# Performance work log

Hardware: AMD Instinct MI355X
Metric: run time of the kernel (lower is better)

The kernel has to match this reference:

```python
import jax, jax.numpy as jnp
import numpy as np

B, T, E, S, D, HG = 16, 1024, 1024, 256, 512, 128
P_MIN, P_MAX, K_MAX, MAX_INNOV, EPS = 1e-6, 10.0, 1.0, 10.0, 1e-6


def setup_inputs() -> dict:
    key = jax.random.key(0)
    ks = jax.random.split(key, 16)
    g = lambda k, shape, fan: jax.random.normal(k, shape, jnp.float32) * np.float32(1.0 / np.sqrt(fan))
    # orthogonal init for the state-transition matrix A
    A = jnp.linalg.qr(jax.random.normal(ks[1], (S, S), jnp.float32))[0]
    return {
        "x": jax.random.normal(ks[0], (B, T, E), jnp.float32),
        "W_in": g(ks[2], (E, D), E), "b_in": jnp.zeros((D,), jnp.float32),
        "W_state": g(ks[3], (D, S), D), "b_state": jnp.zeros((S,), jnp.float32),
        "A": A, "H": g(ks[4], (D, S), D),
        "Q": jnp.full((S,), 0.1, jnp.float32), "R": jnp.full((D,), 0.1, jnp.float32),
        "W_z": g(ks[5], (HG, HG + S), HG + S), "W_r": g(ks[6], (HG, HG + S), HG + S),
        "W_h": g(ks[7], (HG, HG + S), HG + S),
        "b_z": jnp.zeros((HG,), jnp.float32), "b_r": jnp.zeros((HG,), jnp.float32),
        "b_h": jnp.zeros((HG,), jnp.float32),
        "W_out": g(ks[8], (HG, S), HG),
        "W_outp": g(ks[9], (D, E), D), "b_outp": jnp.zeros((E,), jnp.float32),
    }


def reference(x, W_in, b_in, W_state, b_state, A, H, Q, R,
              W_z, W_r, W_h, b_z, b_r, b_h, W_out, W_outp, b_outp):
    # input projection with GELU (Dense(d_inner, activation='gelu'))
    u = jax.nn.gelu(jnp.einsum("bte,ed->btd", x, W_in) + b_in)  # [B,T,D]
    q_sp = jax.nn.softplus(Q)                 # process noise, per state dim
    r_eff = jnp.mean(jax.nn.softplus(R))      # scalar effective measurement noise

    def step(carry, u_t):
        x_est, P, h = carry                   # [B,S], [B,S], [B,HG]
        # 1. state prediction (+ learned control input from measurement)
        x_pred = x_est @ A.T + u_t @ W_state + b_state          # [B,S]
        # 2. covariance prediction with clipping
        P_pred = jnp.clip(P + q_sp, P_MIN, P_MAX)                # [B,S]
        # 3. innovation (clipped for stability)
        y = jnp.clip(u_t - x_pred @ H.T, -MAX_INNOV, MAX_INNOV)  # [B,D]
        # 4. Kalman gain, bounded in [0, k_max]
        K = jnp.clip(P_pred / (P_pred + r_eff + EPS), 0.0, K_MAX)  # [B,S]
        # 5. state update: x_post = x_pred + K * (H^T @ innovation)
        x_post = x_pred + K * (y @ H)                            # [B,S]
        # 6. covariance update
        P_post = jnp.clip(P_pred * (1.0 - K), P_MIN, P_MAX)      # [B,S]
        # GRU gating over posterior state
        hx = jnp.concatenate([h, x_post], axis=-1)               # [B,HG+S]
        zg = jax.nn.sigmoid(hx @ W_z.T + b_z)
        rg = jax.nn.sigmoid(hx @ W_r.T + b_r)
        hc = jnp.tanh(jnp.concatenate([rg * h, x_post], axis=-1) @ W_h.T + b_h)
        h_new = (1.0 - zg) * h + zg * hc                         # [B,HG]
        # neural correction of state via GRU output projection
        x_final = x_post + h_new @ W_out                         # [B,S]
        return (x_final, P_post, h_new), x_final

    x0 = jnp.zeros((x.shape[0], S), x.dtype)
    P0 = jnp.ones((x.shape[0], S), x.dtype)   # identity covariance (diagonal)
    h0 = jnp.zeros((x.shape[0], HG), x.dtype)
    (_, _, _), xs = jax.lax.scan(step, (x0, P0, h0), jnp.swapaxes(u, 0, 1))
    xs = jnp.swapaxes(xs, 0, 1)               # [B,T,S]
    obs = jnp.einsum("bts,ds->btd", xs, H)    # reconstruct observation space
    out = jnp.einsum("btd,de->bte", obs, W_outp) + b_outp
    return out + x                            # residual connection
```

## Files before the change

### kernel.cpp

```cpp
#include <hip/hip_runtime.h>
#include <cstdint>
#include <cstddef>

#define NB 16
#define NT 1024
#define NE 1024
#define NS 256
#define ND 512
#define NH 128
#define T0 16

#define OFF_US   ((size_t)0)
#define OFF_HU   ((size_t)4194304)
#define OFF_U3   ((size_t)8388608)
#define OFF_KT   ((size_t)12582912)
#define OFF_HT   ((size_t)12845056)
#define OFF_AT   ((size_t)12976128)
#define OFF_G    ((size_t)13041664)
#define OFF_IG   ((size_t)13107200)
#define OFF_MINF ((size_t)13172736)
#define OFF_WZT  ((size_t)13238272)
#define OFF_WRT  ((size_t)13287424)
#define OFF_WHT  ((size_t)13336576)
#define OFF_HTWO ((size_t)13385728)
#define OFF_PACK ((size_t)13647872)
#define OFF_XSPK ((size_t)14360576)

#define PK_A   0
#define PK_G   65536
#define PK_M   131072
#define PK_Z   196608
#define PK_R   245760
#define PK_H   294912
#define PK_O   344064
#define PK_WIN 376832
#define PK_WST 901120
#define PK_HM  1032192
#define PK_HTW 1163264


typedef short bf16x8 __attribute__((ext_vector_type(8)));
typedef float f32x4 __attribute__((ext_vector_type(4)));
typedef unsigned int u32x2 __attribute__((ext_vector_type(2)));

#define MFMA(a, b, c) __builtin_amdgcn_mfma_f32_16x16x32_bf16((a), (b), (c), 0, 0, 0)

#define SYNCW() do { \
    __builtin_amdgcn_sched_barrier(0); \
    asm volatile("s_waitcnt lgkmcnt(0)" ::: "memory"); \
    __builtin_amdgcn_s_barrier(); \
    __builtin_amdgcn_sched_barrier(0); \
} while (0)

__device__ __forceinline__ float gelu_tanh(float v) {
    const float c = 0.7978845608028654f;
    float t = tanhf(c * (v + 0.044715f * v * v * v));
    return 0.5f * v * (1.0f + t);
}
__device__ __forceinline__ float softplus_f(float x) {
    if (x > 20.0f) return x;
    return log1pf(expf(x));
}
__device__ __forceinline__ short f2bf_s(float f) {
    unsigned u = __float_as_uint(f);
    u += 0x7fffu + ((u >> 16) & 1u);
    return (short)(u >> 16);
}
__device__ __forceinline__ unsigned pk_bf(float a, float b) {
    return ((unsigned)(unsigned short)f2bf_s(b) << 16) | (unsigned)(unsigned short)f2bf_s(a);
}
__device__ __forceinline__ float exp2_hw(float x) {
    float r; asm("v_exp_f32 %0, %1" : "=v"(r) : "v"(x)); return r;
}
__device__ __forceinline__ float rcp_hw(float x) {
    float r; asm("v_rcp_f32 %0, %1" : "=v"(r) : "v"(x)); return r;
}
__device__ __forceinline__ f32x4 sig4(f32x4 x) {
    f32x4 o;
#pragma unroll
    for (int i = 0; i < 4; ++i)
        o[i] = rcp_hw(1.0f + exp2_hw(-1.442695040888963f * x[i]));
    return o;
}
__device__ __forceinline__ f32x4 tanh4(f32x4 x) {
    f32x4 o;
#pragma unroll
    for (int i = 0; i < 4; ++i) {
        float e = exp2_hw(2.885390081777927f * x[i]);
        o[i] = 1.0f - 2.0f * rcp_hw(e + 1.0f);
    }
    return o;
}
__device__ __forceinline__ void st_bf4(char* base, int stride, int row, int byteoff,
                                       const f32x4& v) {
    u32x2 p;
    p[0] = pk_bf(v[0], v[1]);
    p[1] = pk_bf(v[2], v[3]);
    *(u32x2*)(base + row * stride + byteoff) = p;
}

#define BFRAG(buf, STR, ks) (*(const bf16x8*)((buf) + (l & 15) * (STR) + (ks) * 64 + (l >> 4) * 16))
#define GFRAG(p, fi) (*(const bf16x8*)((p) + ((size_t)(fi) * 64 + l) * 8))
#define LFRAG(buf, fi) (*(const bf16x8*)((buf) + (size_t)(fi) * 1024 + l * 16))

__global__ __launch_bounds__(512) void k_precompute(const float* __restrict__ Q,
                                                    const float* __restrict__ R,
                                                    float* __restrict__ Kt) {
    __shared__ float red[512];
    __shared__ float r_eff_sh;
    const int t = threadIdx.x;
    red[t] = softplus_f(R[t]);
    __syncthreads();
    for (int s = 256; s > 0; s >>= 1) {
        if (t < s) red[t] += red[t + s];
        __syncthreads();
    }
    if (t == 0) r_eff_sh = red[0] / 512.0f;
    __syncthreads();
    const float r_eff = r_eff_sh;
    if (t < NS) {
        const float q = softplus_f(Q[t]);
        float P = 1.0f;
        for (int step = 0; step < NT; ++step) {
            float Pp = fminf(fmaxf(P + q, 1e-6f), 10.0f);
            float K  = fminf(fmaxf(Pp / (Pp + r_eff + 1e-6f), 0.0f), 1.0f);
            Kt[(size_t)step * NS + t] = K;
            P = fminf(fmaxf(Pp * (1.0f - K), 1e-6f), 10.0f);
        }
    }
}

__global__ void k_transpose(const float* __restrict__ in, float* __restrict__ outp,
                            int Rr, int Cc) {
    int i = blockIdx.x * 256 + threadIdx.x;
    if (i < Rr * Cc) {
        int r = i / Cc, c = i % Cc;
        outp[(size_t)c * Rr + r] = in[i];
    }
}

__global__ void k_ig(const float* __restrict__ G, const float* __restrict__ Kt,
                     float* __restrict__ IG) {
    int i = blockIdx.x * 256 + threadIdx.x;
    if (i >= NS * NS) return;
    int r = i >> 8, c = i & 255;
    float kinf = Kt[(size_t)(NT - 1) * NS + c];
    IG[i] = ((r == c) ? 1.0f : 0.0f) - G[i] * kinf;
}

__global__ void k_fuse(const float* __restrict__ us, const float* __restrict__ usG,
                       const float* __restrict__ Hu, const float* __restrict__ Kt,
                       float* __restrict__ u3) {
    int i = blockIdx.x * 256 + threadIdx.x;
    if (i >= NT * NB * NS) return;
    int s = i & 255;
    int tm = i >> 8;
    int m = tm & 15, t = tm >> 4;
    size_t src = ((size_t)m * NT + t) * NS + s;
    float k = Kt[(size_t)t * NS + s];
    u3[i] = us[src] + k * (Hu[src] - usG[src]);
}

__global__ void k_pack(const float* __restrict__ W, short* __restrict__ dst, int K, int N) {
    int f = blockIdx.x * 256 + threadIdx.x;
    if (f >= K * N) return;
    const int j = f & 7, l = (f >> 3) & 63, tile = f >> 9;
    const int KS = K >> 5;
    const int nt = tile / KS, ks = tile - nt * KS;
    const int k = ks * 32 + (l >> 4) * 8 + j;
    const int n = nt * 16 + (l & 15);
    dst[f] = f2bf_s(W[(size_t)k * N + n]);
}

__global__ void k_packA(const float* __restrict__ A, short* __restrict__ dst,
                        int K, int total) {
    int f = blockIdx.x * 256 + threadIdx.x;
    if (f >= total) return;
    const int j = f & 7, l = (f >> 3) & 63, tile = f >> 9;
    const int KS = K >> 5;
    const int mt = tile / KS, ks = tile - mt * KS;
    dst[f] = f2bf_s(A[(size_t)(mt * 16 + (l & 15)) * K + ks * 32 + (l >> 4) * 8 + j]);
}

__global__ __launch_bounds__(256) void k_mm(const short* __restrict__ Apk,
                                            const short* __restrict__ Bpk,
                                            const float* __restrict__ bias,
                                            const float* __restrict__ resid,
                                            float* __restrict__ C,
                                            int N, int K, int act) {
    const int tid = threadIdx.x, w = tid >> 6, l = tid & 63;
    const int KS = K >> 5;
    const int mt = blockIdx.x * 4 + w;
    const int nt0 = blockIdx.y * 8;
    f32x4 acc[8];
#pragma unroll
    for (int j = 0; j < 8; ++j) acc[j] = (f32x4){0.f, 0.f, 0.f, 0.f};
    for (int ks = 0; ks < KS; ++ks) {
        bf16x8 a = *(const bf16x8*)(Apk + ((size_t)(mt * KS + ks) * 64 + l) * 8);
#pragma unroll
        for (int j = 0; j < 8; ++j) {
            bf16x8 b = *(const bf16x8*)(Bpk + ((size_t)(nt0 + j) * KS + ks) * 512 + (size_t)l * 8);
            acc[j] = MFMA(b, a, acc[j]);
        }
    }
    const int m = mt * 16 + (l & 15);
    const int lg = l >> 4;
#pragma unroll
    for (int j = 0; j < 8; ++j) {
        const int n = (nt0 + j) * 16 + lg * 4;
        f32x4 v = acc[j];
        if (bias) v += *(const f32x4*)(bias + n);
        if (act) {
#pragma unroll
            for (int r = 0; r < 4; ++r) v[r] = gelu_tanh(v[r]);
        }
        if (resid) v += *(const f32x4*)(resid + (size_t)m * N + n);
        *(f32x4*)(C + (size_t)m * N + n) = v;
    }
}

__global__ __launch_bounds__(256) void k_gemm(const float* __restrict__ Am,
                                              const float* __restrict__ Bm,
                                              const float* __restrict__ bias,
                                              const float* __restrict__ resid,
                                              float* __restrict__ Cm,
                                              int M, int N, int K, int act) {
    __shared__ __align__(16) float As[16][68];
    __shared__ __align__(16) float Bs[16][68];
    const int tid = threadIdx.x;
    const int bn = blockIdx.x, bm = blockIdx.y;
    const int row0 = bm * 64, col0 = bn * 64;
    const int tx = tid & 15, ty = tid >> 4;
    const int ar = tid >> 2, ac = (tid & 3) << 2;
    const int bk = tid >> 4, bc = (tid & 15) << 2;

    float acc[4][4];
#pragma unroll
    for (int i = 0; i < 4; ++i)
#pragma unroll
        for (int j = 0; j < 4; ++j) acc[i][j] = 0.0f;

    for (int k0 = 0; k0 < K; k0 += 16) {
        float4 av = *(const float4*)(Am + (size_t)(row0 + ar) * K + k0 + ac);
        float4 bv = *(const float4*)(Bm + (size_t)(k0 + bk) * N + col0 + bc);
        As[ac + 0][ar] = av.x; As[ac + 1][ar] = av.y;
        As[ac + 2][ar] = av.z; As[ac + 3][ar] = av.w;
        *(float4*)&Bs[bk][bc] = bv;
        __syncthreads();
#pragma unroll
        for (int kk = 0; kk < 16; ++kk) {
            const float a0 = As[kk][ty * 4 + 0], a1 = As[kk][ty * 4 + 1];
            const float a2 = As[kk][ty * 4 + 2], a3 = As[kk][ty * 4 + 3];
            const float4 b4 = *(const float4*)&Bs[kk][tx * 4];
            acc[0][0] += a0 * b4.x; acc[0][1] += a0 * b4.y; acc[0][2] += a0 * b4.z; acc[0][3] += a0 * b4.w;
            acc[1][0] += a1 * b4.x; acc[1][1] += a1 * b4.y; acc[1][2] += a1 * b4.z; acc[1][3] += a1 * b4.w;
            acc[2][0] += a2 * b4.x; acc[2][1] += a2 * b4.y; acc[2][2] += a2 * b4.z; acc[2][3] += a2 * b4.w;
            acc[3][0] += a3 * b4.x; acc[3][1] += a3 * b4.y; acc[3][2] += a3 * b4.z; acc[3][3] += a3 * b4.w;
        }
        __syncthreads();
    }
#pragma unroll
    for (int i = 0; i < 4; ++i) {
        const int r = row0 + ty * 4 + i;
#pragma unroll
        for (int j = 0; j < 4; ++j) {
            const int c = col0 + tx * 4 + j;
            float v = acc[i][j];
            if (bias) v += bias[c];
            if (act) v = gelu_tanh(v);
            if (resid) v += resid[(size_t)r * N + c];
            Cm[(size_t)r * N + c] = v;
        }
    }
}

#define XE_STR 528
#define HB_STR 272

__global__ __launch_bounds__(512, 2) void k_scan_mfma(
    const short* __restrict__ pM, const short* __restrict__ pA, const short* __restrict__ pG,
    const short* __restrict__ pZ, const short* __restrict__ pR, const short* __restrict__ pH,
    const short* __restrict__ pO,
    const float* __restrict__ bz, const float* __restrict__ br, const float* __restrict__ bh,
    const float* __restrict__ us, const float* __restrict__ Hu, const float* __restrict__ u3,
    const float* __restrict__ Kt, float* __restrict__ xs)
{
    __shared__ __align__(16) char XE[16 * XE_STR];
    __shared__ __align__(16) char XT[16 * XE_STR];
    __shared__ __align__(16) char HBs[16 * HB_STR];
    __shared__ __align__(16) char RGs[16 * HB_STR];
    __shared__ __align__(16) char WHH[96 * 1024];

    const int tid = threadIdx.x, w = tid >> 6, l = tid & 63;
    const int m = l & 15, lg = l >> 4;
    const int c0 = 32 * w + 4 * lg;
    const int cg = 16 * w + 4 * lg;

    for (int i = tid; i < (16 * XE_STR) / 4; i += 512) ((int*)XE)[i] = 0;
    for (int i = tid; i < (16 * HB_STR) / 4; i += 512) ((int*)HBs)[i] = 0;
    for (int i = tid; i < 6144; i += 512) ((int4*)WHH)[i] = ((const int4*)pH)[i];

    const f32x4 bzv = *(const f32x4*)(bz + cg);
    const f32x4 brv = *(const f32x4*)(br + cg);
    const f32x4 bhv = *(const f32x4*)(bh + cg);
    f32x4 hFr = {0.f, 0.f, 0.f, 0.f};
    __syncthreads();

    for (int t = 0; t < T0; ++t) {
        const float* usb = us + ((size_t)m * NT + t) * NS;
        const float* hub = Hu + ((size_t)m * NT + t) * NS;
        const float* ktb = Kt + (size_t)t * NS;
        f32x4 us0 = *(const f32x4*)(usb + c0), us1 = *(const f32x4*)(usb + c0 + 16);
        f32x4 hu0 = *(const f32x4*)(hub + c0), hu1 = *(const f32x4*)(hub + c0 + 16);
        f32x4 kv0 = *(const f32x4*)(ktb + c0), kv1 = *(const f32x4*)(ktb + c0 + 16);
        f32x4 p0 = {0.f,0.f,0.f,0.f}, p1 = {0.f,0.f,0.f,0.f};
#pragma unroll
        for (int ks = 0; ks < 8; ++ks) {
            bf16x8 xe = BFRAG(XE, XE_STR, ks);
            p0 = MFMA(GFRAG(pA, (2 * w + 0) * 8 + ks), xe, p0);
            p1 = MFMA(GFRAG(pA, (2 * w + 1) * 8 + ks), xe, p1);
        }
        p0 += us0; p1 += us1;
        st_bf4(XT, XE_STR, m, c0 * 2, p0);
        st_bf4(XT, XE_STR, m, (c0 + 16) * 2, p1);
        SYNCW();
        f32x4 g0 = {0.f,0.f,0.f,0.f}, g1 = {0.f,0.f,0.f,0.f};
#pragma unroll
        for (int ks = 0; ks < 8; ++ks) {
            bf16x8 xt = BFRAG(XT, XE_STR, ks);
            g0 = MFMA(GFRAG(pG, (2 * w + 0) * 8 + ks), xt, g0);
            g1 = MFMA(GFRAG(pG, (2 * w + 1) * 8 + ks), xt, g1);
        }
        f32x4 xq0 = p0 + kv0 * (hu0 - g0);
        f32x4 xq1 = p1 + kv1 * (hu1 - g1);
        st_bf4(XE, XE_STR, m, c0 * 2, xq0);
        st_bf4(XE, XE_STR, m, (c0 + 16) * 2, xq1);
        SYNCW();
        f32x4 za = bzv, ra = brv, hx = bhv;
#pragma unroll
        for (int ks = 0; ks < 4; ++ks) {
            bf16x8 hb = BFRAG(HBs, HB_STR, ks);
            za = MFMA(GFRAG(pZ, w * 12 + ks), hb, za);
            ra = MFMA(GFRAG(pR, w * 12 + ks), hb, ra);
        }
#pragma unroll
        for (int ks = 0; ks < 8; ++ks) {
            bf16x8 xef = BFRAG(XE, XE_STR, ks);
            za = MFMA(GFRAG(pZ, w * 12 + 4 + ks), xef, za);
            ra = MFMA(GFRAG(pR, w * 12 + 4 + ks), xef, ra);
            hx = MFMA(GFRAG(pH, w * 12 + 4 + ks), xef, hx);
        }
        f32x4 z = sig4(za), r = sig4(ra), rg = r * hFr;
        st_bf4(RGs, HB_STR, m, cg * 2, rg);
        SYNCW();
        f32x4 hc = hx;
#pragma unroll
        for (int ks = 0; ks < 4; ++ks)
            hc = MFMA(GFRAG(pH, w * 12 + ks), BFRAG(RGs, HB_STR, ks), hc);
        f32x4 hcv = tanh4(hc);
        f32x4 hn = hFr + z * (hcv - hFr);
        hFr = hn;
        st_bf4(HBs, HB_STR, m, cg * 2, hn);
        SYNCW();
#pragma unroll
        for (int ks = 0; ks < 4; ++ks) {
            bf16x8 hb2 = BFRAG(HBs, HB_STR, ks);
            xq0 = MFMA(GFRAG(pO, (2 * w + 0) * 4 + ks), hb2, xq0);
            xq1 = MFMA(GFRAG(pO, (2 * w + 1) * 4 + ks), hb2, xq1);
        }
        st_bf4(XE, XE_STR, m, c0 * 2, xq0);
        st_bf4(XE, XE_STR, m, (c0 + 16) * 2, xq1);
        {
            float* xb = xs + ((size_t)m * NT + t) * NS;
            *(f32x4*)(xb + c0) = xq0;
            *(f32x4*)(xb + c0 + 16) = xq1;
        }
        SYNCW();
    }

    bf16x8 rM0[8], rM1[8], rZx[8], rRx[8], rZh[4], rRh[4], rO0[4], rO1[4];
#pragma unroll
    for (int ks = 0; ks < 8; ++ks) {
        rM0[ks] = GFRAG(pM, (2 * w + 0) * 8 + ks);
        rM1[ks] = GFRAG(pM, (2 * w + 1) * 8 + ks);
        rZx[ks] = GFRAG(pZ, w * 12 + 4 + ks);
        rRx[ks] = GFRAG(pR, w * 12 + 4 + ks);
    }
#pragma unroll
    for (int ks = 0; ks < 4; ++ks) {
        rZh[ks] = GFRAG(pZ, w * 12 + ks);
        rRh[ks] = GFRAG(pR, w * 12 + ks);
        rO0[ks] = GFRAG(pO, (2 * w + 0) * 4 + ks);
        rO1[ks] = GFRAG(pO, (2 * w + 1) * 4 + ks);
    }

    f32x4 zh = bzv, rh = brv;
#pragma unroll
    for (int ks = 0; ks < 4; ++ks) {
        bf16x8 hb = BFRAG(HBs, HB_STR, ks);
        zh = MFMA(rZh[ks], hb, zh);
        rh = MFMA(rRh[ks], hb, rh);
    }

    for (int t = T0; t < NT; ++t) {
        const float* ubase = u3 + ((size_t)(t * NB) + m) * NS;
        f32x4 cu0 = *(const f32x4*)(ubase + c0);
        f32x4 cu1 = *(const f32x4*)(ubase + c0 + 16);

        f32x4 xq0 = {0.f,0.f,0.f,0.f}, xq1 = {0.f,0.f,0.f,0.f};
#pragma unroll
        for (int ks = 0; ks < 8; ++ks) {
            bf16x8 xe = BFRAG(XE, XE_STR, ks);
            xq0 = MFMA(rM0[ks], xe, xq0);
            xq1 = MFMA(rM1[ks], xe, xq1);
        }
        xq0 += cu0; xq1 += cu1;
        st_bf4(XT, XE_STR, m, c0 * 2, xq0);
        st_bf4(XT, XE_STR, m, (c0 + 16) * 2, xq1);
        SYNCW();
        f32x4 za = zh, ra = rh, hx = bhv;
#pragma unroll
        for (int ks = 0; ks < 8; ++ks) {
            bf16x8 xt = BFRAG(XT, XE_STR, ks);
            za = MFMA(rZx[ks], xt, za);
            ra = MFMA(rRx[ks], xt, ra);
            hx = MFMA(LFRAG(WHH, w * 12 + 4 + ks), xt, hx);
        }
        f32x4 z = sig4(za), r = sig4(ra), rg = r * hFr;
        st_bf4(RGs, HB_STR, m, cg * 2, rg);
        SYNCW();
        f32x4 hc = hx;
#pragma unroll
        for (int ks = 0; ks < 4; ++ks)
            hc = MFMA(LFRAG(WHH, w * 12 + ks), BFRAG(RGs, HB_STR, ks), hc);
        f32x4 hcv = tanh4(hc);
        f32x4 hn = hFr + z * (hcv - hFr);
        hFr = hn;
        st_bf4(HBs, HB_STR, m, cg * 2, hn);
        SYNCW();
        f32x4 zhN = bzv, rhN = brv;
#pragma unroll
        for (int ks = 0; ks < 4; ++ks) {
            bf16x8 hb2 = BFRAG(HBs, HB_STR, ks);
            xq0 = MFMA(rO0[ks], hb2, xq0);
            xq1 = MFMA(rO1[ks], hb2, xq1);
            zhN = MFMA(rZh[ks], hb2, zhN);
            rhN = MFMA(rRh[ks], hb2, rhN);
        }
        st_bf4(XE, XE_STR, m, c0 * 2, xq0);
        st_bf4(XE, XE_STR, m, (c0 + 16) * 2, xq1);
        {
            float* xb = xs + ((size_t)m * NT + t) * NS;
            *(f32x4*)(xb + c0) = xq0;
            *(f32x4*)(xb + c0 + 16) = xq1;
        }
        zh = zhN; rh = rhN;
        SYNCW();
    }
}

extern "C" void kernel_launch(void* const* d_in, const int* in_sizes, int n_in,
                              void* d_out, int out_size, void* d_ws, size_t ws_size,
                              hipStream_t stream) {
    (void)in_sizes; (void)n_in; (void)out_size; (void)ws_size;
    const float* x       = (const float*)d_in[0];
    const float* W_in    = (const float*)d_in[1];
    const float* b_in    = (const float*)d_in[2];
    const float* W_state = (const float*)d_in[3];
    const float* b_state = (const float*)d_in[4];
    const float* A       = (const float*)d_in[5];
    const float* H       = (const float*)d_in[6];
    const float* Q       = (const float*)d_in[7];
    const float* R       = (const float*)d_in[8];
    const float* W_z     = (const float*)d_in[9];
    const float* W_r     = (const float*)d_in[10];
    const float* W_h     = (const float*)d_in[11];
    const float* b_z     = (const float*)d_in[12];
    const float* b_r     = (const float*)d_in[13];
    const float* b_h     = (const float*)d_in[14];
    const float* W_out   = (const float*)d_in[15];
    const float* W_outp  = (const float*)d_in[16];
    const float* b_outp  = (const float*)d_in[17];
    float* out = (float*)d_out;
    float* w = (float*)d_ws;

    float* us   = w + OFF_US;
    float* Hu   = w + OFF_HU;
    float* u3   = w + OFF_U3;
    float* Kt   = w + OFF_KT;
    float* Ht   = w + OFF_HT;
    float* At   = w + OFF_AT;
    float* G    = w + OFF_G;
    float* IG   = w + OFF_IG;
    float* Minf = w + OFF_MINF;
    float* Wzt  = w + OFF_WZT;
    float* Wrt  = w + OFF_WRT;
    float* Wht  = w + OFF_WHT;
    float* HtWo = w + OFF_HTWO;
    short* pk   = (short*)(w + OFF_PACK);
    short* xs_pk = (short*)(w + OFF_XSPK);

    short* x_pk  = (short*)out;
    short* u_pk  = (short*)out;
    short* us_pk = (short*)out;
    float* usG   = out + (size_t)4194304;
    float* u     = out + (size_t)8388608;
    float* xs    = out + (size_t)8388608;

    const int M = NB * NT;

    hipLaunchKernelGGL(k_precompute, dim3(1), dim3(512), 0, stream, Q, R, Kt);
    hipLaunchKernelGGL(k_transpose, dim3((NS * NS + 255) / 256), dim3(256), 0, stream, A, At, NS, NS);
    hipLaunchKernelGGL(k_transpose, dim3((ND * NS + 255) / 256), dim3(256), 0, stream, H, Ht, ND, NS);
    hipLaunchKernelGGL(k_transpose, dim3((NH * 384 + 255) / 256), dim3(256), 0, stream, W_z, Wzt, NH, 384);
    hipLaunchKernelGGL(k_transpose, dim3((NH * 384 + 255) / 256), dim3(256), 0, stream, W_r, Wrt, NH, 384);
    hipLaunchKernelGGL(k_transpose, dim3((NH * 384 + 255) / 256), dim3(256), 0, stream, W_h, Wht, NH, 384);
    hipLaunchKernelGGL(k_gemm, dim3(NS / 64, NS / 64), dim3(256), 0, stream,
                       Ht, H, nullptr, nullptr, G, NS, NS, ND, 0);
    hipLaunchKernelGGL(k_gemm, dim3(NE / 64, NS / 64), dim3(256), 0, stream,
                       Ht, W_outp, nullptr, nullptr, HtWo, NS, NE, ND, 0);
    hipLaunchKernelGGL(k_ig, dim3(256), dim3(256), 0, stream, G, Kt, IG);
    hipLaunchKernelGGL(k_gemm, dim3(NS / 64, NS / 64), dim3(256), 0, stream,
                       At, IG, nullptr, nullptr, Minf, NS, NS, NS, 0);
    hipLaunchKernelGGL(k_pack, dim3((NS * NS + 255) / 256), dim3(256), 0, stream, At, pk + PK_A, NS, NS);
    hipLaunchKernelGGL(k_pack, dim3((NS * NS + 255) / 256), dim3(256), 0, stream, G, pk + PK_G, NS, NS);
    hipLaunchKernelGGL(k_pack, dim3((NS * NS + 255) / 256), dim3(256), 0, stream, Minf, pk + PK_M, NS, NS);
    hipLaunchKernelGGL(k_pack, dim3((384 * NH + 255) / 256), dim3(256), 0, stream, Wzt, pk + PK_Z, 384, NH);
    hipLaunchKernelGGL(k_pack, dim3((384 * NH + 255) / 256), dim3(256), 0, stream, Wrt, pk + PK_R, 384, NH);
    hipLaunchKernelGGL(k_pack, dim3((384 * NH + 255) / 256), dim3(256), 0, stream, Wht, pk + PK_H, 384, NH);
    hipLaunchKernelGGL(k_pack, dim3((NH * NS + 255) / 256), dim3(256), 0, stream, W_out, pk + PK_O, NH, NS);
    hipLaunchKernelGGL(k_pack, dim3((NE * ND + 255) / 256), dim3(256), 0, stream, W_in, pk + PK_WIN, NE, ND);
    hipLaunchKernelGGL(k_pack, dim3((ND * NS + 255) / 256), dim3(256), 0, stream, W_state, pk + PK_WST, ND, NS);
    hipLaunchKernelGGL(k_pack, dim3((ND * NS + 255) / 256), dim3(256), 0, stream, H, pk + PK_HM, ND, NS);
    hipLaunchKernelGGL(k_pack, dim3((NS * NE + 255) / 256), dim3(256), 0, stream, HtWo, pk + PK_HTW, NS, NE);
    hipLaunchKernelGGL(k_packA, dim3((M * NE) / 256), dim3(256), 0, stream, x, x_pk, NE, M * NE);
    hipLaunchKernelGGL(k_mm, dim3(M / 64, ND / 128), dim3(256), 0, stream,
                       x_pk, pk + PK_WIN, b_in, nullptr, u, ND, NE, 1);
    hipLaunchKernelGGL(k_packA, dim3((M * ND) / 256), dim3(256), 0, stream, u, u_pk, ND, M * ND);
    hipLaunchKernelGGL(k_mm, dim3(M / 64, NS / 128), dim3(256), 0, stream,
                       u_pk, pk + PK_WST, b_state, nullptr, us, NS, ND, 0);
    hipLaunchKernelGGL(k_mm, dim3(M / 64, NS / 128), dim3(256), 0, stream,
                       u_pk, pk + PK_HM, nullptr, nullptr, Hu, NS, ND, 0);
    hipLaunchKernelGGL(k_packA, dim3((M * NS) / 256), dim3(256), 0, stream, us, us_pk, NS, M * NS);
    hipLaunchKernelGGL(k_mm, dim3(M / 64, NS / 128), dim3(256), 0, stream,
                       us_pk, pk + PK_G, nullptr, nullptr, usG, NS, NS, 0);
    hipLaunchKernelGGL(k_fuse, dim3((NT * NB * NS) / 256), dim3(256), 0, stream,
                       us, usG, Hu, Kt, u3);
    hipLaunchKernelGGL(k_scan_mfma, dim3(1), dim3(512), 0, stream,
                       pk + PK_M, pk + PK_A, pk + PK_G, pk + PK_Z, pk + PK_R, pk + PK_H,
                       pk + PK_O,
                       b_z, b_r, b_h, us, Hu, u3, Kt, xs);
    hipLaunchKernelGGL(k_packA, dim3((M * NS) / 256), dim3(256), 0, stream, xs, xs_pk, NS, M * NS);
    hipLaunchKernelGGL(k_mm, dim3(M / 64, NE / 128), dim3(256), 0, stream,
                       xs_pk, pk + PK_HTW, b_outp, x, out, NE, NS, 0);
}
```

Baseline: 3.267 ms.

## Fuse bf16 activation packing into GEMM loads and prefetch scan inputs

Removes the separate k_packA passes. The GEMM kernel now reads fp32 activations directly and converts them to bf16 fragments in registers, which saves several full-size read/write passes over the activation buffers. In the sequential scan, the recurrent W_h fragments move from LDS into registers, the LDS buffer shrinks, and the next timestep's u3 input is prefetched one step ahead. The costs are extra fp32 load bandwidth and conversion work inside the GEMM loop, plus higher register pressure in the scan kernel. The xs buffer is relocated to the workspace.

```diff
diff --git a/kernel.cpp b/kernel.cpp
--- a/kernel.cpp
+++ b/kernel.cpp
@@ -24,7 +24,6 @@
 #define OFF_WHT  ((size_t)13336576)
 #define OFF_HTWO ((size_t)13385728)
 #define OFF_PACK ((size_t)13647872)
-#define OFF_XSPK ((size_t)14360576)
 
 #define PK_A   0
 #define PK_G   65536
@@ -172,17 +171,7 @@
     dst[f] = f2bf_s(W[(size_t)k * N + n]);
 }
 
-__global__ void k_packA(const float* __restrict__ A, short* __restrict__ dst,
-                        int K, int total) {
-    int f = blockIdx.x * 256 + threadIdx.x;
-    if (f >= total) return;
-    const int j = f & 7, l = (f >> 3) & 63, tile = f >> 9;
-    const int KS = K >> 5;
-    const int mt = tile / KS, ks = tile - mt * KS;
-    dst[f] = f2bf_s(A[(size_t)(mt * 16 + (l & 15)) * K + ks * 32 + (l >> 4) * 8 + j]);
-}
-
-__global__ __launch_bounds__(256) void k_mm(const short* __restrict__ Apk,
+__global__ __launch_bounds__(256) void k_mm(const float* __restrict__ Af,
                                             const short* __restrict__ Bpk,
                                             const float* __restrict__ bias,
                                             const float* __restrict__ resid,
@@ -192,15 +181,21 @@
     const int KS = K >> 5;
     const int mt = blockIdx.x * 4 + w;
     const int nt0 = blockIdx.y * 8;
+    const float* arow = Af + (size_t)(mt * 16 + (l & 15)) * K + ((l >> 4) * 8);
     f32x4 acc[8];
 #pragma unroll
     for (int j = 0; j < 8; ++j) acc[j] = (f32x4){0.f, 0.f, 0.f, 0.f};
     for (int ks = 0; ks < KS; ++ks) {
-        bf16x8 a = *(const bf16x8*)(Apk + ((size_t)(mt * KS + ks) * 64 + l) * 8);
+        const float* ap = arow + ks * 32;
+        f32x4 a0 = *(const f32x4*)ap;
+        f32x4 a1 = *(const f32x4*)(ap + 4);
+        union { bf16x8 v; unsigned u[4]; } au;
+        au.u[0] = pk_bf(a0[0], a0[1]); au.u[1] = pk_bf(a0[2], a0[3]);
+        au.u[2] = pk_bf(a1[0], a1[1]); au.u[3] = pk_bf(a1[2], a1[3]);
 #pragma unroll
         for (int j = 0; j < 8; ++j) {
             bf16x8 b = *(const bf16x8*)(Bpk + ((size_t)(nt0 + j) * KS + ks) * 512 + (size_t)l * 8);
-            acc[j] = MFMA(b, a, acc[j]);
+            acc[j] = MFMA(b, au.v, acc[j]);
         }
     }
     const int m = mt * 16 + (l & 15);
@@ -289,7 +284,7 @@
     __shared__ __align__(16) char XT[16 * XE_STR];
     __shared__ __align__(16) char HBs[16 * HB_STR];
     __shared__ __align__(16) char RGs[16 * HB_STR];
-    __shared__ __align__(16) char WHH[96 * 1024];
+    __shared__ __align__(16) char WHH[64 * 1024];
 
     const int tid = threadIdx.x, w = tid >> 6, l = tid & 63;
     const int m = l & 15, lg = l >> 4;
@@ -298,7 +293,11 @@
 
     for (int i = tid; i < (16 * XE_STR) / 4; i += 512) ((int*)XE)[i] = 0;
     for (int i = tid; i < (16 * HB_STR) / 4; i += 512) ((int*)HBs)[i] = 0;
-    for (int i = tid; i < 6144; i += 512) ((int4*)WHH)[i] = ((const int4*)pH)[i];
+    for (int i = tid; i < 4096; i += 512) {
+        int fi = i >> 6, ln = i & 63;
+        int wv = fi >> 3, ks = fi & 7;
+        ((int4*)WHH)[i] = *(const int4*)(pH + ((size_t)(wv * 12 + 4 + ks) * 64 + ln) * 8);
+    }
 
     const f32x4 bzv = *(const f32x4*)(bz + cg);
     const f32x4 brv = *(const f32x4*)(br + cg);
@@ -378,7 +377,7 @@
         SYNCW();
     }
 
-    bf16x8 rM0[8], rM1[8], rZx[8], rRx[8], rZh[4], rRh[4], rO0[4], rO1[4];
+    bf16x8 rM0[8], rM1[8], rZx[8], rRx[8], rZh[4], rRh[4], rO0[4], rO1[4], rHh[4];
 #pragma unroll
     for (int ks = 0; ks < 8; ++ks) {
         rM0[ks] = GFRAG(pM, (2 * w + 0) * 8 + ks);
@@ -392,6 +391,7 @@
         rRh[ks] = GFRAG(pR, w * 12 + ks);
         rO0[ks] = GFRAG(pO, (2 * w + 0) * 4 + ks);
         rO1[ks] = GFRAG(pO, (2 * w + 1) * 4 + ks);
+        rHh[ks] = GFRAG(pH, w * 12 + ks);
     }
 
     f32x4 zh = bzv, rh = brv;
@@ -402,10 +402,14 @@
         rh = MFMA(rRh[ks], hb, rh);
     }
 
+    f32x4 cu0 = *(const f32x4*)(u3 + (size_t)T0 * (NB * NS) + (size_t)m * NS + c0);
+    f32x4 cu1 = *(const f32x4*)(u3 + (size_t)T0 * (NB * NS) + (size_t)m * NS + c0 + 16);
+
     for (int t = T0; t < NT; ++t) {
-        const float* ubase = u3 + ((size_t)(t * NB) + m) * NS;
-        f32x4 cu0 = *(const f32x4*)(ubase + c0);
-        f32x4 cu1 = *(const f32x4*)(ubase + c0 + 16);
+        const int tn = (t + 1 < NT) ? (t + 1) : t;
+        const float* ubn = u3 + (size_t)tn * (NB * NS) + (size_t)m * NS;
+        f32x4 nx0 = *(const f32x4*)(ubn + c0);
+        f32x4 nx1 = *(const f32x4*)(ubn + c0 + 16);
 
         f32x4 xq0 = {0.f,0.f,0.f,0.f}, xq1 = {0.f,0.f,0.f,0.f};
 #pragma unroll
@@ -424,7 +428,7 @@
             bf16x8 xt = BFRAG(XT, XE_STR, ks);
             za = MFMA(rZx[ks], xt, za);
             ra = MFMA(rRx[ks], xt, ra);
-            hx = MFMA(LFRAG(WHH, w * 12 + 4 + ks), xt, hx);
+            hx = MFMA(LFRAG(WHH, w * 8 + ks), xt, hx);
         }
         f32x4 z = sig4(za), r = sig4(ra), rg = r * hFr;
         st_bf4(RGs, HB_STR, m, cg * 2, rg);
@@ -432,7 +436,7 @@
         f32x4 hc = hx;
 #pragma unroll
         for (int ks = 0; ks < 4; ++ks)
-            hc = MFMA(LFRAG(WHH, w * 12 + ks), BFRAG(RGs, HB_STR, ks), hc);
+            hc = MFMA(rHh[ks], BFRAG(RGs, HB_STR, ks), hc);
         f32x4 hcv = tanh4(hc);
         f32x4 hn = hFr + z * (hcv - hFr);
         hFr = hn;
@@ -455,6 +459,7 @@
             *(f32x4*)(xb + c0 + 16) = xq1;
         }
         zh = zhN; rh = rhN;
+        cu0 = nx0; cu1 = nx1;
         SYNCW();
     }
 }
@@ -498,14 +503,10 @@
     float* Wht  = w + OFF_WHT;
     float* HtWo = w + OFF_HTWO;
     short* pk   = (short*)(w + OFF_PACK);
-    short* xs_pk = (short*)(w + OFF_XSPK);
-
-    short* x_pk  = (short*)out;
-    short* u_pk  = (short*)out;
-    short* us_pk = (short*)out;
-    float* usG   = out + (size_t)4194304;
-    float* u     = out + (size_t)8388608;
-    float* xs    = out + (size_t)8388608;
+
+    float* xs  = w + OFF_US;
+    float* usG = out + (size_t)4194304;
+    float* u   = out + (size_t)8388608;
 
     const int M = NB * NT;
 
@@ -533,24 +534,20 @@
     hipLaunchKernelGGL(k_pack, dim3((ND * NS + 255) / 256), dim3(256), 0, stream, W_state, pk + PK_WST, ND, NS);
     hipLaunchKernelGGL(k_pack, dim3((ND * NS + 255) / 256), dim3(256), 0, stream, H, pk + PK_HM, ND, NS);
     hipLaunchKernelGGL(k_pack, dim3((NS * NE + 255) / 256), dim3(256), 0, stream, HtWo, pk + PK_HTW, NS, NE);
-    hipLaunchKernelGGL(k_packA, dim3((M * NE) / 256), dim3(256), 0, stream, x, x_pk, NE, M * NE);
     hipLaunchKernelGGL(k_mm, dim3(M / 64, ND / 128), dim3(256), 0, stream,
-                       x_pk, pk + PK_WIN, b_in, nullptr, u, ND, NE, 1);
-    hipLaunchKernelGGL(k_packA, dim3((M * ND) / 256), dim3(256), 0, stream, u, u_pk, ND, M * ND);
+                       x, pk + PK_WIN, b_in, nullptr, u, ND, NE, 1);
     hipLaunchKernelGGL(k_mm, dim3(M / 64, NS / 128), dim3(256), 0, stream,
-                       u_pk, pk + PK_WST, b_state, nullptr, us, NS, ND, 0);
+                       u, pk + PK_WST, b_state, nullptr, us, NS, ND, 0);
     hipLaunchKernelGGL(k_mm, dim3(M / 64, NS / 128), dim3(256), 0, stream,
-                       u_pk, pk + PK_HM, nullptr, nullptr, Hu, NS, ND, 0);
-    hipLaunchKernelGGL(k_packA, dim3((M * NS) / 256), dim3(256), 0, stream, us, us_pk, NS, M * NS);
+                       u, pk + PK_HM, nullptr, nullptr, Hu, NS, ND, 0);
     hipLaunchKernelGGL(k_mm, dim3(M / 64, NS / 128), dim3(256), 0, stream,
-                       us_pk, pk + PK_G, nullptr, nullptr, usG, NS, NS, 0);
+                       us, pk + PK_G, nullptr, nullptr, usG, NS, NS, 0);
     hipLaunchKernelGGL(k_fuse, dim3((NT * NB * NS) / 256), dim3(256), 0, stream,
                        us, usG, Hu, Kt, u3);
     hipLaunchKernelGGL(k_scan_mfma, dim3(1), dim3(512), 0, stream,
                        pk + PK_M, pk + PK_A, pk + PK_G, pk + PK_Z, pk + PK_R, pk + PK_H,
                        pk + PK_O,
                        b_z, b_r, b_h, us, Hu, u3, Kt, xs);
-    hipLaunchKernelGGL(k_packA, dim3((M * NS) / 256), dim3(256), 0, stream, xs, xs_pk, NS, M * NS);
     hipLaunchKernelGGL(k_mm, dim3(M / 64, NE / 128), dim3(256), 0, stream,
-                       xs_pk, pk + PK_HTW, b_outp, x, out, NE, NS, 0);
-}
+                       xs, pk + PK_HTW, b_outp, x, out, NE, NS, 0);
+}
```

New measurement: 3.778 ms. +15.6%, slower.
